# Optimization experiments

Hardware: AMD Instinct MI355X
Metric: run time of the kernel (lower is better)

Reference implementation:

```python
import jax, jax.numpy as jnp
import numpy as np

NEG_SLOPE = 0.01  # nn.LeakyReLU default

def _leaky(x):
    return jnp.where(x >= 0, x, NEG_SLOPE * x)

def setup_inputs() -> dict:
    key = jax.random.key(0)
    ks = jax.random.split(key, 8)
    in_ch = 64
    B, H, W = 8, 256, 256
    x = jax.random.normal(ks[0], (B, 2 * in_ch, H, W), dtype=jnp.float32)
    dims = [(64, 128), (32, 64), (16, 32), (8, 16), (4, 8), (2, 4), (1, 2)]
    inp = {"x": x}
    for i, (o, c) in enumerate(dims):
        # kaiming_normal_ fan_out, relu: std = sqrt(2 / fan_out), fan_out = o*1*1
        std = np.sqrt(2.0 / o).astype(np.float32)
        inp[f"w{i+1}"] = jax.random.normal(ks[i + 1], (o, c), dtype=jnp.float32) * std
    return inp

def reference(x, w1, w2, w3, w4, w5, w6, w7):
    # Each 1x1 conv (bias-free) is a per-pixel matmul over channels.
    h = x
    for w in (w1, w2, w3, w4, w5, w6):
        h = _leaky(jnp.einsum('bchw,oc->bohw', h, w))
    out = jnp.einsum('bchw,oc->bohw', h, w7)  # final conv, no activation
    return out
```

## Files before the change

### kernel.cpp

```cpp
#include <hip/hip_runtime.h>


#define NEG_SLOPE 0.01f
constexpr int HW = 65536;

typedef __attribute__((ext_vector_type(8))) short bf16x8;
typedef __attribute__((ext_vector_type(4))) float f32x4;
typedef __attribute__((ext_vector_type(2))) float f32x2;

__device__ __forceinline__ float leaky(float v) { return v >= 0.f ? v : NEG_SLOPE * v; }

__device__ __forceinline__ short f2b(float f) {
    unsigned u = __float_as_uint(f);
    u += 0x7fffu + ((u >> 16) & 1u);
    return (short)(u >> 16);
}
__device__ __forceinline__ unsigned pk2(float a, float b) {
    return (unsigned)(unsigned short)f2b(a) | ((unsigned)(unsigned short)f2b(b) << 16);
}

__device__ __forceinline__ bf16x8 loadA(const float* __restrict__ wsrc, int C, int m, int k) {
    f32x4 lo = *(const f32x4*)(wsrc + m * C + k);
    f32x4 hi = *(const f32x4*)(wsrc + m * C + k + 4);
    union { bf16x8 v; unsigned u[4]; } r;
    r.u[0] = pk2(lo[0], lo[1]); r.u[1] = pk2(lo[2], lo[3]);
    r.u[2] = pk2(hi[0], hi[1]); r.u[3] = pk2(hi[2], hi[3]);
    return r.v;
}

__device__ __forceinline__ void async_cp16(const float* g, float* l) {
    __builtin_amdgcn_global_load_lds((const __attribute__((address_space(1))) unsigned*)g,
                                     (__attribute__((address_space(3))) unsigned*)l,
                                     16, 0, 0);
}

__global__ __launch_bounds__(256, 2) void fused_staged_kernel(
    const float* __restrict__ x,
    const float* __restrict__ w1, const float* __restrict__ w2,
    const float* __restrict__ w3, const float* __restrict__ w4,
    const float* __restrict__ w5, const float* __restrict__ w6,
    const float* __restrict__ w7, float* __restrict__ out) {
    __shared__ float lds_x[2][32 * 128];
    __shared__ unsigned long long lds_un[4][544];
    __shared__ float lds_tw[176];

    const int tid = threadIdx.x;
    if (tid < 128)      lds_tw[tid] = w4[tid];
    else if (tid < 160) lds_tw[tid] = w5[tid - 128];
    else if (tid < 168) lds_tw[tid] = w6[tid - 160];
    else if (tid < 170) lds_tw[tid] = w7[tid - 168];

    const int w    = tid >> 6;
    const int lane = tid & 63;
    const int n    = lane & 15;
    const int q    = lane >> 4;
    const int half = lane >> 5;
    const int pl   = lane & 31;

    const int px0   = blockIdx.x * 128;
    const int batch = px0 >> 16;
    const int pin   = px0 & (HW - 1);
    const float* xg = x + (size_t)batch * 128 * HW + pin;

#pragma unroll
    for (int i = 0; i < 4; ++i) {
        int cp = w * 8 + 2 * i;
        const float* g = xg + (size_t)(cp + half) * HW + pl * 4;
        async_cp16(g, &lds_x[0][cp * 128]);
    }

    bf16x8 a1[4][4];
#pragma unroll
    for (int Mt = 0; Mt < 4; ++Mt)
#pragma unroll
        for (int kc = 0; kc < 4; ++kc)
            a1[Mt][kc] = loadA(w1, 128, Mt * 16 + n, kc * 32 + q * 8);
    bf16x8 a2[2][2];
#pragma unroll
    for (int Mt = 0; Mt < 2; ++Mt)
#pragma unroll
        for (int kc = 0; kc < 2; ++kc)
            a2[Mt][kc] = loadA(w2, 64, Mt * 16 + n, kc * 32 + q * 8);
    bf16x8 a3 = loadA(w3, 32, n, q * 8);

    __syncthreads();

    f32x4 acc1[4][2];
#pragma unroll
    for (int Mt = 0; Mt < 4; ++Mt)
#pragma unroll
        for (int Nt = 0; Nt < 2; ++Nt) acc1[Mt][Nt] = (f32x4){0.f, 0.f, 0.f, 0.f};

#pragma unroll
    for (int kc = 0; kc < 4; ++kc) {
        if (kc < 3) {
#pragma unroll
            for (int i = 0; i < 4; ++i) {
                int cp = w * 8 + 2 * i;
                const float* g = xg + (size_t)((kc + 1) * 32 + cp + half) * HW + pl * 4;
                async_cp16(g, &lds_x[(kc + 1) & 1][cp * 128]);
            }
        }
        const float* xb = &lds_x[kc & 1][0];
#pragma unroll
        for (int Nt = 0; Nt < 2; ++Nt) {
            float t[8];
#pragma unroll
            for (int j = 0; j < 8; ++j)
                t[j] = xb[(q * 8 + j) * 128 + w * 32 + Nt * 16 + n];
            union { bf16x8 v; unsigned u[4]; } b;
            b.u[0] = pk2(t[0], t[1]); b.u[1] = pk2(t[2], t[3]);
            b.u[2] = pk2(t[4], t[5]); b.u[3] = pk2(t[6], t[7]);
#pragma unroll
            for (int Mt = 0; Mt < 4; ++Mt)
                acc1[Mt][Nt] = __builtin_amdgcn_mfma_f32_16x16x32_bf16(a1[Mt][kc], b.v, acc1[Mt][Nt], 0, 0, 0);
        }
        if (kc < 3) __syncthreads();
    }

    short* h1 = (short*)&lds_un[w][0];
#pragma unroll
    for (int Mt = 0; Mt < 4; ++Mt)
#pragma unroll
        for (int Nt = 0; Nt < 2; ++Nt) {
            int px = Nt * 16 + n;
            uint2 v;
            v.x = pk2(leaky(acc1[Mt][Nt][0]), leaky(acc1[Mt][Nt][1]));
            v.y = pk2(leaky(acc1[Mt][Nt][2]), leaky(acc1[Mt][Nt][3]));
            *(uint2*)(h1 + px * 68 + Mt * 16 + q * 4) = v;
        }

    f32x4 acc2[2][2];
#pragma unroll
    for (int Mt = 0; Mt < 2; ++Mt)
#pragma unroll
        for (int Nt = 0; Nt < 2; ++Nt) acc2[Mt][Nt] = (f32x4){0.f, 0.f, 0.f, 0.f};
#pragma unroll
    for (int Nt = 0; Nt < 2; ++Nt)
#pragma unroll
        for (int kc = 0; kc < 2; ++kc) {
            int off = (Nt * 16 + n) * 68 + kc * 32 + q * 8;
            uint2 lo = *(const uint2*)(h1 + off);
            uint2 hi = *(const uint2*)(h1 + off + 4);
            union { bf16x8 v; unsigned u[4]; } b;
            b.u[0] = lo.x; b.u[1] = lo.y; b.u[2] = hi.x; b.u[3] = hi.y;
#pragma unroll
            for (int Mt = 0; Mt < 2; ++Mt)
                acc2[Mt][Nt] = __builtin_amdgcn_mfma_f32_16x16x32_bf16(a2[Mt][kc], b.v, acc2[Mt][Nt], 0, 0, 0);
        }

    short* h2 = (short*)&lds_un[w][0];
#pragma unroll
    for (int Mt = 0; Mt < 2; ++Mt)
#pragma unroll
        for (int Nt = 0; Nt < 2; ++Nt) {
            int px = Nt * 16 + n;
            uint2 v;
            v.x = pk2(leaky(acc2[Mt][Nt][0]), leaky(acc2[Mt][Nt][1]));
            v.y = pk2(leaky(acc2[Mt][Nt][2]), leaky(acc2[Mt][Nt][3]));
            *(uint2*)(h2 + px * 36 + Mt * 16 + q * 4) = v;
        }

    f32x4 acc3[2];
#pragma unroll
    for (int Nt = 0; Nt < 2; ++Nt) {
        int off = (Nt * 16 + n) * 36 + q * 8;
        uint2 lo = *(const uint2*)(h2 + off);
        uint2 hi = *(const uint2*)(h2 + off + 4);
        union { bf16x8 v; unsigned u[4]; } b;
        b.u[0] = lo.x; b.u[1] = lo.y; b.u[2] = hi.x; b.u[3] = hi.y;
        f32x4 zero = {0.f, 0.f, 0.f, 0.f};
        acc3[Nt] = __builtin_amdgcn_mfma_f32_16x16x32_bf16(a3, b.v, zero, 0, 0, 0);
    }

    float* h3 = (float*)&lds_un[w][0];
#pragma unroll
    for (int Nt = 0; Nt < 2; ++Nt) {
        int px = Nt * 16 + n;
        f32x2 va = {leaky(acc3[Nt][0]), leaky(acc3[Nt][1])};
        f32x2 vb = {leaky(acc3[Nt][2]), leaky(acc3[Nt][3])};
        *(f32x2*)(h3 + px * 18 + q * 4)     = va;
        *(f32x2*)(h3 + px * 18 + q * 4 + 2) = vb;
    }

    float hh[16];
#pragma unroll
    for (int c = 0; c < 16; ++c) hh[c] = h3[pl * 18 + c];

    float g4[8];
#pragma unroll
    for (int o = 0; o < 8; ++o) {
        float a = 0.f;
#pragma unroll
        for (int c = 0; c < 16; ++c) a = fmaf(lds_tw[o * 16 + c], hh[c], a);
        g4[o] = leaky(a);
    }
    float g5[4];
#pragma unroll
    for (int o = 0; o < 4; ++o) {
        float a = 0.f;
#pragma unroll
        for (int c = 0; c < 8; ++c) a = fmaf(lds_tw[128 + o * 8 + c], g4[c], a);
        g5[o] = leaky(a);
    }
    float g6[2];
#pragma unroll
    for (int o = 0; o < 2; ++o) {
        float a = 0.f;
#pragma unroll
        for (int c = 0; c < 4; ++c) a = fmaf(lds_tw[160 + o * 4 + c], g5[c], a);
        g6[o] = leaky(a);
    }
    float res = fmaf(lds_tw[168], g6[0], lds_tw[169] * g6[1]);
    if (lane < 32) out[px0 + w * 32 + pl] = res;
}

extern "C" void kernel_launch(void* const* d_in, const int* in_sizes, int n_in,
                              void* d_out, int out_size, void* d_ws, size_t ws_size,
                              hipStream_t stream) {
    const float* x  = (const float*)d_in[0];
    const float* w1 = (const float*)d_in[1];
    const float* w2 = (const float*)d_in[2];
    const float* w3 = (const float*)d_in[3];
    const float* w4 = (const float*)d_in[4];
    const float* w5 = (const float*)d_in[5];
    const float* w6 = (const float*)d_in[6];
    const float* w7 = (const float*)d_in[7];
    float* out = (float*)d_out;

    const int P = 8 * 256 * 256;
    fused_staged_kernel<<<P / 128, 256, 0, stream>>>(x, w1, w2, w3, w4, w5, w6, w7, out);
}
```

Baseline: 404.2 us.

## Give each wave its own x slab with all loads issued upfront and vmcnt waits

```diff
diff --git a/kernel.cpp b/kernel.cpp
--- a/kernel.cpp
+++ b/kernel.cpp
@@ -8,15 +8,13 @@
 typedef __attribute__((ext_vector_type(4))) float f32x4;
 typedef __attribute__((ext_vector_type(2))) float f32x2;
 
-__device__ __forceinline__ float leaky(float v) { return v >= 0.f ? v : NEG_SLOPE * v; }
-
-__device__ __forceinline__ short f2b(float f) {
-    unsigned u = __float_as_uint(f);
-    u += 0x7fffu + ((u >> 16) & 1u);
-    return (short)(u >> 16);
-}
+__device__ __forceinline__ float leaky(float v) { return fmaxf(v, v * NEG_SLOPE); }
+
 __device__ __forceinline__ unsigned pk2(float a, float b) {
-    return (unsigned)(unsigned short)f2b(a) | ((unsigned)(unsigned short)f2b(b) << 16);
+    __bf16 ba = (__bf16)a, bb = (__bf16)b;
+    unsigned short ua = __builtin_bit_cast(unsigned short, ba);
+    unsigned short ub = __builtin_bit_cast(unsigned short, bb);
+    return (unsigned)ua | ((unsigned)ub << 16);
 }
 
 __device__ __forceinline__ bf16x8 loadA(const float* __restrict__ wsrc, int C, int m, int k) {
@@ -34,14 +32,15 @@
                                      16, 0, 0);
 }
 
-__global__ __launch_bounds__(256, 2) void fused_staged_kernel(
+__device__ __forceinline__ void cfence() { asm volatile("" ::: "memory"); }
+
+__global__ __launch_bounds__(256, 2) void fused_wavepipe_kernel(
     const float* __restrict__ x,
     const float* __restrict__ w1, const float* __restrict__ w2,
     const float* __restrict__ w3, const float* __restrict__ w4,
     const float* __restrict__ w5, const float* __restrict__ w6,
     const float* __restrict__ w7, float* __restrict__ out) {
-    __shared__ float lds_x[2][32 * 128];
-    __shared__ unsigned long long lds_un[4][544];
+    __shared__ float lds_x[4][4096];
     __shared__ float lds_tw[176];
 
     const int tid = threadIdx.x;
@@ -54,20 +53,26 @@
     const int lane = tid & 63;
     const int n    = lane & 15;
     const int q    = lane >> 4;
-    const int half = lane >> 5;
     const int pl   = lane & 31;
 
     const int px0   = blockIdx.x * 128;
     const int batch = px0 >> 16;
     const int pin   = px0 & (HW - 1);
-    const float* xg = x + (size_t)batch * 128 * HW + pin;
-
-#pragma unroll
-    for (int i = 0; i < 4; ++i) {
-        int cp = w * 8 + 2 * i;
-        const float* g = xg + (size_t)(cp + half) * HW + pl * 4;
-        async_cp16(g, &lds_x[0][cp * 128]);
-    }
+    const float* xg = x + (size_t)batch * 128 * HW + pin + w * 32;
+
+    float* Xw = &lds_x[w][0];
+
+    __syncthreads();
+
+    const int r  = lane >> 3;
+    const int s4 = (lane & 7) * 4;
+    const float* xgr = xg + (size_t)r * HW;
+
+#pragma unroll
+    for (int i = 0; i < 4; ++i)
+        async_cp16(xgr + (size_t)(i * 8) * HW + (s4 ^ ((i & 3) * 8)), Xw + i * 256);
+    cfence();
+    __builtin_amdgcn_sched_barrier(0);
 
     bf16x8 a1[4][4];
 #pragma unroll
@@ -82,8 +87,14 @@
         for (int kc = 0; kc < 2; ++kc)
             a2[Mt][kc] = loadA(w2, 64, Mt * 16 + n, kc * 32 + q * 8);
     bf16x8 a3 = loadA(w3, 32, n, q * 8);
-
-    __syncthreads();
+    cfence();
+    __builtin_amdgcn_sched_barrier(0);
+
+#pragma unroll
+    for (int i = 4; i < 16; ++i)
+        async_cp16(xgr + (size_t)(i * 8) * HW + (s4 ^ ((i & 3) * 8)), Xw + i * 256);
+    cfence();
+    __builtin_amdgcn_sched_barrier(0);
 
     f32x4 acc1[4][2];
 #pragma unroll
@@ -91,23 +102,22 @@
 #pragma unroll
         for (int Nt = 0; Nt < 2; ++Nt) acc1[Mt][Nt] = (f32x4){0.f, 0.f, 0.f, 0.f};
 
+    const int pq = q * 8;
 #pragma unroll
     for (int kc = 0; kc < 4; ++kc) {
-        if (kc < 3) {
-#pragma unroll
-            for (int i = 0; i < 4; ++i) {
-                int cp = w * 8 + 2 * i;
-                const float* g = xg + (size_t)((kc + 1) * 32 + cp + half) * HW + pl * 4;
-                async_cp16(g, &lds_x[(kc + 1) & 1][cp * 128]);
-            }
-        }
-        const float* xb = &lds_x[kc & 1][0];
+        if      (kc == 0) asm volatile("s_waitcnt vmcnt(12)" ::: "memory");
+        else if (kc == 1) asm volatile("s_waitcnt vmcnt(8)"  ::: "memory");
+        else if (kc == 2) asm volatile("s_waitcnt vmcnt(4)"  ::: "memory");
+        else              asm volatile("s_waitcnt vmcnt(0)"  ::: "memory");
+        __builtin_amdgcn_sched_barrier(0);
+        const float* xb = Xw + kc * 1024;
 #pragma unroll
         for (int Nt = 0; Nt < 2; ++Nt) {
+            const int pxsw = (Nt * 16 + n) ^ pq;
             float t[8];
 #pragma unroll
             for (int j = 0; j < 8; ++j)
-                t[j] = xb[(q * 8 + j) * 128 + w * 32 + Nt * 16 + n];
+                t[j] = xb[(pq + j) * 32 + pxsw];
             union { bf16x8 v; unsigned u[4]; } b;
             b.u[0] = pk2(t[0], t[1]); b.u[1] = pk2(t[2], t[3]);
             b.u[2] = pk2(t[4], t[5]); b.u[3] = pk2(t[6], t[7]);
@@ -115,10 +125,10 @@
             for (int Mt = 0; Mt < 4; ++Mt)
                 acc1[Mt][Nt] = __builtin_amdgcn_mfma_f32_16x16x32_bf16(a1[Mt][kc], b.v, acc1[Mt][Nt], 0, 0, 0);
         }
-        if (kc < 3) __syncthreads();
-    }
-
-    short* h1 = (short*)&lds_un[w][0];
+    }
+    cfence();
+
+    short* h1 = (short*)Xw;
 #pragma unroll
     for (int Mt = 0; Mt < 4; ++Mt)
 #pragma unroll
@@ -129,6 +139,7 @@
             v.y = pk2(leaky(acc1[Mt][Nt][2]), leaky(acc1[Mt][Nt][3]));
             *(uint2*)(h1 + px * 68 + Mt * 16 + q * 4) = v;
         }
+    cfence();
 
     f32x4 acc2[2][2];
 #pragma unroll
@@ -148,8 +159,9 @@
             for (int Mt = 0; Mt < 2; ++Mt)
                 acc2[Mt][Nt] = __builtin_amdgcn_mfma_f32_16x16x32_bf16(a2[Mt][kc], b.v, acc2[Mt][Nt], 0, 0, 0);
         }
-
-    short* h2 = (short*)&lds_un[w][0];
+    cfence();
+
+    short* h2 = (short*)Xw;
 #pragma unroll
     for (int Mt = 0; Mt < 2; ++Mt)
 #pragma unroll
@@ -160,6 +172,7 @@
             v.y = pk2(leaky(acc2[Mt][Nt][2]), leaky(acc2[Mt][Nt][3]));
             *(uint2*)(h2 + px * 36 + Mt * 16 + q * 4) = v;
         }
+    cfence();
 
     f32x4 acc3[2];
 #pragma unroll
@@ -172,8 +185,9 @@
         f32x4 zero = {0.f, 0.f, 0.f, 0.f};
         acc3[Nt] = __builtin_amdgcn_mfma_f32_16x16x32_bf16(a3, b.v, zero, 0, 0, 0);
     }
-
-    float* h3 = (float*)&lds_un[w][0];
+    cfence();
+
+    float* h3 = (float*)Xw;
 #pragma unroll
     for (int Nt = 0; Nt < 2; ++Nt) {
         int px = Nt * 16 + n;
@@ -182,6 +196,7 @@
         *(f32x2*)(h3 + px * 18 + q * 4)     = va;
         *(f32x2*)(h3 + px * 18 + q * 4 + 2) = vb;
     }
+    cfence();
 
     float hh[16];
 #pragma unroll
@@ -229,5 +244,5 @@
     float* out = (float*)d_out;
 
     const int P = 8 * 256 * 256;
-    fused_staged_kernel<<<P / 128, 256, 0, stream>>>(x, w1, w2, w3, w4, w5, w6, w7, out);
-}
+    fused_wavepipe_kernel<<<P / 128, 256, 0, stream>>>(x, w1, w2, w3, w4, w5, w6, w7, out);
+}
```

After: 398.9 us. No clear change (-1.3%).
